# Kernel optimization log

Hardware: AMD Instinct MI355X
Metric: run time of the kernel (lower is better)

## Reference

```python
import jax, jax.numpy as jnp
import numpy as np

G = 64  # fixed grid size hardcoded in the torch module

def setup_inputs() -> dict:
    key = jax.random.key(0)
    ks = jax.random.split(key, 12)
    N, H = 500000, 256
    s = lambda fan_in: 1.0 / np.sqrt(fan_in)
    return {
        "positions": jax.random.normal(ks[0], (N, 3), jnp.float32) * 2.0,
        "grid_points": jax.random.normal(ks[1], (G, 3), jnp.float32) * 2.0,
        "W1": jax.random.normal(ks[2], (3, 64), jnp.float32) * s(3),
        "b1": jnp.zeros((64,), jnp.float32),
        "W2": jax.random.normal(ks[3], (64, 128), jnp.float32) * s(64),
        "b2": jnp.zeros((128,), jnp.float32),
        "W3": jax.random.normal(ks[4], (128, H), jnp.float32) * s(128),
        "b3": jnp.zeros((H,), jnp.float32),
        "Wn1": jax.random.normal(ks[5], (H, H), jnp.float32) * s(H),
        "bn1": jnp.zeros((H,), jnp.float32),
        "Wn2": jax.random.normal(ks[6], (H, H), jnp.float32) * s(H),
        "bn2": jnp.zeros((H,), jnp.float32),
        "Wh1": jax.random.normal(ks[7], (4, H, 128), jnp.float32) * s(H),
        "bh1": jnp.zeros((4, 128), jnp.float32),
        "Wh2": jax.random.normal(ks[8], (4, 128, 1), jnp.float32) * s(128),
        "bh2": jnp.zeros((4, 1), jnp.float32),
    }

def reference(positions, grid_points, W1, b1, W2, b2, W3, b3,
              Wn1, bn1, Wn2, bn2, Wh1, bh1, Wh2, bh2):
    # crystal_encoder: per-atom MLP 3 -> 64 -> 128 -> 256 over ALL N atoms
    h = jax.nn.relu(positions @ W1 + b1)
    h = jax.nn.relu(h @ W2 + b2)
    feat = h @ W3 + b3                                   # [N, H]

    # _map_crystal_to_grid: only the first min(N, 64) atoms are mapped.
    pos64 = positions[:G]                                # [64, 3]
    d2 = jnp.sum((pos64[:, None, :] - grid_points[None, :, :]) ** 2, axis=-1)
    idx = jnp.argmin(d2, axis=-1)                        # [64] nearest grid point per atom
    winner = jnp.full((G,), -1, jnp.int32).at[idx].max(jnp.arange(G, dtype=jnp.int32))
    grid_feats = jnp.where(winner[:, None] >= 0,
                           feat[jnp.clip(winner, 0)], 0.0)  # [64, H]

    # TetrahedralAGINetwork (per-node MLP, channels-first output convention)
    x = grid_feats[None]                                 # [1, 64, H]
    y = jax.nn.relu(x @ Wn1 + bn1) @ Wn2 + bn2           # [1, 64, H]
    agg = jnp.mean(jnp.swapaxes(y, 1, 2), axis=-1)       # mean over nodes -> [1, H]

    # 4 property heads, batched: [4, 1, 1] -> [4] (order: band_gap,
    # elastic_modulus, thermal_conductivity, dielectric_constant)
    h1 = jax.nn.relu(jnp.einsum('bc,kcd->kbd', agg, Wh1) + bh1[:, None, :])
    props = jnp.einsum('kbd,kdo->kbo', h1, Wh2) + bh2[:, None, :]
    return props.reshape(4)
```

## Files before the change

### kernel.cpp

```cpp
#include <hip/hip_runtime.h>


__device__ __forceinline__ void async_cp16(const float* g, float* l) {
    __builtin_amdgcn_global_load_lds(
        (const __attribute__((address_space(1))) void*)g,
        (__attribute__((address_space(3))) void*)l, 16, 0, 0);
}
__device__ __forceinline__ void stage_contig(const float* g, float* l, int nfloats, int tid) {
    const int lane = tid & 63, wv = tid >> 6;
    const int ninst = nfloats >> 8;
    for (int i = wv; i < ninst; i += 4)
        async_cp16(g + i*256 + lane*4, l + i*256);
}
__device__ __forceinline__ void stage_slice32(const float* g, float* l, int ld, int j0, int nrows, int tid) {
    const int lane = tid & 63, wv = tid >> 6;
    const int r = lane >> 3, c4 = (lane & 7) << 2;
    const int ninst = nrows >> 3;
    for (int i = wv; i < ninst; i += 4)
        async_cp16(g + (i*8 + r)*ld + j0 + c4, l + i*256);
}
__device__ __forceinline__ void stage_slice16(const float* g, float* l, int ld, int j0, int nrows, int tid) {
    const int lane = tid & 63, wv = tid >> 6;
    const int r = lane >> 2, c4 = (lane & 3) << 2;
    const int ninst = nrows >> 4;
    for (int i = wv; i < ninst; i += 4)
        async_cp16(g + (i*16 + r)*ld + j0 + c4, l + i*256);
}

__global__ __launch_bounds__(256) void k1a_gf(
    const float* __restrict__ positions, const float* __restrict__ grid_pts,
    const float* __restrict__ W1, const float* __restrict__ b1,
    const float* __restrict__ W2, const float* __restrict__ b2,
    const float* __restrict__ W3, const float* __restrict__ b3,
    float* __restrict__ gf_ws)
{
    __shared__ __align__(16) float w3s[128*32];
    __shared__ float pos_s[192], grid_s[192], w1_s[192], b1_s[64];
    __shared__ int   idx_s[64], win_s[8];
    __shared__ __align__(16) float h1s[8*64];
    __shared__ __align__(16) float h2s[8*128];

    const int tid = threadIdx.x;
    const int blk = blockIdx.x;
    const int bg  = blk >> 3;
    const int j0  = (blk & 7) * 32;

    if (tid < 192) { pos_s[tid] = positions[tid]; grid_s[tid] = grid_pts[tid]; w1_s[tid] = W1[tid]; }
    if (tid >= 192) b1_s[tid - 192] = b1[tid - 192];
    const float bb2 = b2[tid & 127];
    __syncthreads();

    stage_slice32(W3, w3s, 256, j0, 128, tid);
    if (tid < 64) {
        const float px = pos_s[tid*3], py = pos_s[tid*3+1], pz = pos_s[tid*3+2];
        float best = 3.4e38f; int bi = 0;
        for (int g = 0; g < 64; ++g) {
            const float dx = px - grid_s[g*3];
            const float dy = py - grid_s[g*3+1];
            const float dz = pz - grid_s[g*3+2];
            const float d2 = dx*dx + dy*dy + dz*dz;
            if (d2 < best) { best = d2; bi = g; }
        }
        idx_s[tid] = bi;
    }
    __syncthreads();
    if (tid < 8) {
        const int g = bg*8 + tid;
        int m = -1;
        for (int i = 0; i < 64; ++i) if (idx_s[i] == g) m = i;
        win_s[tid] = m;
    }
    __syncthreads();

    #pragma unroll
    for (int u = 0; u < 2; ++u) {
        const int e  = tid + u*256;
        const int lr = e >> 6, kk = e & 63;
        int r = win_s[lr]; if (r < 0) r = 0;
        const float acc = b1_s[kk] + pos_s[r*3]*w1_s[kk] + pos_s[r*3+1]*w1_s[64+kk]
                                   + pos_s[r*3+2]*w1_s[128+kk];
        h1s[lr*64 + kk] = fmaxf(acc, 0.f);
    }
    __syncthreads();

    {
        const int d = tid & 127, t0 = tid >> 7;
        float acc[4];
        #pragma unroll
        for (int m = 0; m < 4; ++m) acc[m] = bb2;
        for (int kc = 0; kc < 64; kc += 16) {
            float w[16];
            #pragma unroll
            for (int u = 0; u < 16; ++u) w[u] = W2[(kc+u)*128 + d];
            #pragma unroll
            for (int u = 0; u < 16; u += 4) {
                #pragma unroll
                for (int m = 0; m < 4; ++m) {
                    const float4 h4 = *(const float4*)&h1s[(t0 + 2*m)*64 + kc + u];
                    acc[m] += h4.x*w[u] + h4.y*w[u+1] + h4.z*w[u+2] + h4.w*w[u+3];
                }
            }
        }
        #pragma unroll
        for (int m = 0; m < 4; ++m)
            h2s[(t0 + 2*m)*128 + d] = fmaxf(acc[m], 0.f);
    }
    __syncthreads();

    {
        const int t = tid >> 5, jl = tid & 31;
        float ag = 0.f;
        for (int dc = 0; dc < 128; dc += 16) {
            float w[16];
            #pragma unroll
            for (int u = 0; u < 16; ++u) w[u] = w3s[(dc+u)*32 + jl];
            #pragma unroll
            for (int u = 0; u < 16; u += 4) {
                const float4 h4 = *(const float4*)&h2s[t*128 + dc + u];
                ag += h4.x*w[u] + h4.y*w[u+1] + h4.z*w[u+2] + h4.w*w[u+3];
            }
        }
        const float bb3 = b3[j0 + jl];
        gf_ws[(bg*8 + t)*256 + j0 + jl] = (win_s[t] >= 0) ? (ag + bb3) : 0.f;
    }
}

__global__ __launch_bounds__(256) void k1b_tpart(
    const float* __restrict__ Wn1, const float* __restrict__ bn1,
    const float* __restrict__ gf_ws, float* __restrict__ tpart_ws)
{
    __shared__ __align__(16) float wn1_s[256*16];
    __shared__ __align__(16) float gf_s[8*256];
    __shared__ float r_s[128];

    const int tid = threadIdx.x;
    const int bg  = blockIdx.x >> 4;
    const int j0  = (blockIdx.x & 15) * 16;
    stage_slice16(Wn1, wn1_s, 256, j0, 256, tid);
    stage_contig(gf_ws + bg*8*256, gf_s, 8*256, tid);

    const int jl = tid & 15, t = tid >> 4;
    const float bb = bn1[j0 + jl];
    __syncthreads();

    if (t < 8) {
        float acc = bb;
        for (int cc = 0; cc < 256; cc += 32) {
            float w[32];
            #pragma unroll
            for (int u = 0; u < 32; ++u) w[u] = wn1_s[(cc+u)*16 + jl];
            #pragma unroll
            for (int u = 0; u < 32; u += 4) {
                const float4 g4 = *(const float4*)&gf_s[t*256 + cc + u];
                acc += g4.x*w[u] + g4.y*w[u+1] + g4.z*w[u+2] + g4.w*w[u+3];
            }
        }
        r_s[t*16 + jl] = fmaxf(acc, 0.f);
    }
    __syncthreads();
    if (t == 0) {
        float ps = 0.f;
        #pragma unroll
        for (int tt = 0; tt < 8; ++tt) ps += r_s[tt*16 + jl];
        tpart_ws[bg*256 + j0 + jl] = ps;
    }
}

__global__ __launch_bounds__(256) void k2_agg(
    const float* __restrict__ Wn2, const float* __restrict__ bn2,
    const float* __restrict__ tpart_ws, float* __restrict__ agg_ws,
    unsigned int* __restrict__ cnts)
{
    __shared__ __align__(16) float wn2_s[256*8];
    __shared__ __align__(16) float tp_s[2048];
    __shared__ __align__(16) float tbar_s[256];

    const int tid = threadIdx.x;
    const int j0a = blockIdx.x * 8;

    if (blockIdx.x == 0 && tid == 0) cnts[0] = 0u;
    {
        const int lane = tid & 63, wv = tid >> 6;
        const int r = lane >> 1, c4 = (lane & 1) << 2;
        for (int i = wv; i < 8; i += 4)
            async_cp16(Wn2 + (i*32 + r)*256 + j0a + c4, wn2_s + i*256);
    }
    stage_contig(tpart_ws, tp_s, 2048, tid);
    __syncthreads();

    {
        float tb = 0.f;
        #pragma unroll
        for (int q = 0; q < 8; ++q) tb += tp_s[q*256 + tid];
        tbar_s[tid] = tb * (1.f/64.f);
    }
    __syncthreads();

    if (tid < 8) {
        float acc = bn2[j0a + tid];
        for (int jc = 0; jc < 256; jc += 32) {
            float w[32];
            #pragma unroll
            for (int u = 0; u < 32; ++u) w[u] = wn2_s[(jc+u)*8 + tid];
            #pragma unroll
            for (int u = 0; u < 32; u += 4) {
                const float4 t4 = *(const float4*)&tbar_s[jc + u];
                acc += t4.x*w[u] + t4.y*w[u+1] + t4.z*w[u+2] + t4.w*w[u+3];
            }
        }
        agg_ws[j0a + tid] = acc;
    }
}

__global__ __launch_bounds__(256) void k34_h1out(
    const float* __restrict__ Wh1, const float* __restrict__ bh1,
    const float* __restrict__ Wh2, const float* __restrict__ bh2,
    const float* __restrict__ agg_ws, float* __restrict__ h1h_ws,
    unsigned int* __restrict__ cnts, float* __restrict__ out)
{
    __shared__ __align__(16) float whs[256*32];
    __shared__ __align__(16) float agg_s[256];
    __shared__ int last_s;

    const int tid = threadIdx.x;
    const int k   = blockIdx.x >> 2;
    const int d0  = (blockIdx.x & 3) * 32;

    stage_slice32(Wh1 + k*32768, whs, 128, d0, 256, tid);
    agg_s[tid] = agg_ws[tid];
    __syncthreads();

    if (tid < 32) {
        const int dl = tid;
        float a = bh1[k*128 + d0 + dl];
        for (int cc = 0; cc < 256; cc += 16) {
            float wa[16];
            #pragma unroll
            for (int u = 0; u < 16; ++u) wa[u] = whs[(cc+u)*32 + dl];
            #pragma unroll
            for (int u = 0; u < 16; u += 4) {
                const float4 a4 = *(const float4*)&agg_s[cc + u];
                a += a4.x*wa[u] + a4.y*wa[u+1] + a4.z*wa[u+2] + a4.w*wa[u+3];
            }
        }
        h1h_ws[k*128 + d0 + dl] = fmaxf(a, 0.f);
    }
    __threadfence();
    __syncthreads();
    if (tid == 0) {
        const unsigned old = __hip_atomic_fetch_add(
            &cnts[0], 1u, __ATOMIC_ACQ_REL, __HIP_MEMORY_SCOPE_AGENT);
        last_s = (old == 15u) ? 1 : 0;
    }
    __syncthreads();
    if (last_s && tid < 4) {
        const int kk = tid;
        float a = bh2[kk];
        for (int d = 0; d < 128; ++d)
            a += h1h_ws[kk*128 + d] * Wh2[kk*128 + d];
        out[kk] = a;
    }
}

extern "C" void kernel_launch(void* const* d_in, const int* in_sizes, int n_in,
                              void* d_out, int out_size, void* d_ws, size_t ws_size,
                              hipStream_t stream) {
    const float* positions = (const float*)d_in[0];
    const float* grid      = (const float*)d_in[1];
    const float* W1  = (const float*)d_in[2];
    const float* b1  = (const float*)d_in[3];
    const float* W2  = (const float*)d_in[4];
    const float* b2  = (const float*)d_in[5];
    const float* W3  = (const float*)d_in[6];
    const float* b3  = (const float*)d_in[7];
    const float* Wn1 = (const float*)d_in[8];
    const float* bn1 = (const float*)d_in[9];
    const float* Wn2 = (const float*)d_in[10];
    const float* bn2 = (const float*)d_in[11];
    const float* Wh1 = (const float*)d_in[12];
    const float* bh1 = (const float*)d_in[13];
    const float* Wh2 = (const float*)d_in[14];
    const float* bh2 = (const float*)d_in[15];
    float* out = (float*)d_out;

    char* ws = (char*)d_ws;
    float* gf_ws    = (float*)(ws + 0);
    float* tpart_ws = (float*)(ws + 65536);
    float* agg_ws   = (float*)(ws + 73728);
    float* h1h_ws   = (float*)(ws + 74752);
    unsigned int* cnts = (unsigned int*)(ws + 76800);

    hipLaunchKernelGGL(k1a_gf,    dim3(64),  dim3(256), 0, stream,
                       positions, grid, W1, b1, W2, b2, W3, b3, gf_ws);
    hipLaunchKernelGGL(k1b_tpart, dim3(128), dim3(256), 0, stream,
                       Wn1, bn1, gf_ws, tpart_ws);
    hipLaunchKernelGGL(k2_agg,    dim3(32),  dim3(256), 0, stream,
                       Wn2, bn2, tpart_ws, agg_ws, cnts);
    hipLaunchKernelGGL(k34_h1out, dim3(16),  dim3(256), 0, stream,
                       Wh1, bh1, Wh2, bh2, agg_ws, h1h_ws, cnts, out);
}
```

Before: 104.1 us.

## Fuse four stage kernels into one persistent kernel with atomic counter barriers

Replaces the four separate kernel launches with a single 240-block kernel. Blocks are partitioned by index into the four stages, and each stage waits on a global atomic counter published by the stage before it. Weight slices are prefetched into LDS before each wait, so weight loading overlaps the upstream stage and three launch gaps go away. It adds a memset launch to reset the counters. Correctness relies on every block being co-resident, and a spin guard breaks out of the wait after a bounded number of iterations, which could let a stage read stale data.

```diff
diff --git a/kernel.cpp b/kernel.cpp
--- a/kernel.cpp
+++ b/kernel.cpp
@@ -27,238 +27,263 @@
         async_cp16(g + (i*16 + r)*ld + j0 + c4, l + i*256);
 }
 
-__global__ __launch_bounds__(256) void k1a_gf(
+#define SPIN_GUARD (1u << 22)
+__device__ __forceinline__ void wait_cnt(unsigned int* p, unsigned int target) {
+    unsigned int g = 0;
+    while (__hip_atomic_load(p, __ATOMIC_ACQUIRE, __HIP_MEMORY_SCOPE_AGENT) < target) {
+        if (++g > SPIN_GUARD) break;
+    }
+}
+
+__global__ __launch_bounds__(256) void mega(
     const float* __restrict__ positions, const float* __restrict__ grid_pts,
     const float* __restrict__ W1, const float* __restrict__ b1,
     const float* __restrict__ W2, const float* __restrict__ b2,
     const float* __restrict__ W3, const float* __restrict__ b3,
-    float* __restrict__ gf_ws)
+    const float* __restrict__ Wn1, const float* __restrict__ bn1,
+    const float* __restrict__ Wn2, const float* __restrict__ bn2,
+    const float* __restrict__ Wh1, const float* __restrict__ bh1,
+    const float* __restrict__ Wh2, const float* __restrict__ bh2,
+    float* __restrict__ gf_ws, float* __restrict__ tpart_ws,
+    float* __restrict__ agg_ws, float* __restrict__ h1h_ws,
+    unsigned int* __restrict__ cnts, float* __restrict__ out)
 {
-    __shared__ __align__(16) float w3s[128*32];
-    __shared__ float pos_s[192], grid_s[192], w1_s[192], b1_s[64];
-    __shared__ int   idx_s[64], win_s[8];
-    __shared__ __align__(16) float h1s[8*64];
-    __shared__ __align__(16) float h2s[8*128];
-
     const int tid = threadIdx.x;
     const int blk = blockIdx.x;
-    const int bg  = blk >> 3;
-    const int j0  = (blk & 7) * 32;
-
-    if (tid < 192) { pos_s[tid] = positions[tid]; grid_s[tid] = grid_pts[tid]; w1_s[tid] = W1[tid]; }
-    if (tid >= 192) b1_s[tid - 192] = b1[tid - 192];
-    const float bb2 = b2[tid & 127];
-    __syncthreads();
-
-    stage_slice32(W3, w3s, 256, j0, 128, tid);
-    if (tid < 64) {
-        const float px = pos_s[tid*3], py = pos_s[tid*3+1], pz = pos_s[tid*3+2];
-        float best = 3.4e38f; int bi = 0;
-        for (int g = 0; g < 64; ++g) {
-            const float dx = px - grid_s[g*3];
-            const float dy = py - grid_s[g*3+1];
-            const float dz = pz - grid_s[g*3+2];
-            const float d2 = dx*dx + dy*dy + dz*dz;
-            if (d2 < best) { best = d2; bi = g; }
-        }
-        idx_s[tid] = bi;
-    }
-    __syncthreads();
-    if (tid < 8) {
-        const int g = bg*8 + tid;
-        int m = -1;
-        for (int i = 0; i < 64; ++i) if (idx_s[i] == g) m = i;
-        win_s[tid] = m;
-    }
-    __syncthreads();
-
-    #pragma unroll
-    for (int u = 0; u < 2; ++u) {
-        const int e  = tid + u*256;
-        const int lr = e >> 6, kk = e & 63;
-        int r = win_s[lr]; if (r < 0) r = 0;
-        const float acc = b1_s[kk] + pos_s[r*3]*w1_s[kk] + pos_s[r*3+1]*w1_s[64+kk]
-                                   + pos_s[r*3+2]*w1_s[128+kk];
-        h1s[lr*64 + kk] = fmaxf(acc, 0.f);
-    }
-    __syncthreads();
+
+    if (blk < 64) {
+        __shared__ __align__(16) float w3s[128*32];
+        __shared__ float pos_s[192], grid_s[192], w1_s[192], b1_s[64];
+        __shared__ int   idx_s[64], win_s[8];
+        __shared__ __align__(16) float h1s[8*64];
+        __shared__ __align__(16) float h2s[8*128];
+
+        const int bg = blk >> 3;
+        const int j0 = (blk & 7) * 32;
+
+        if (tid < 192) { pos_s[tid] = positions[tid]; grid_s[tid] = grid_pts[tid]; w1_s[tid] = W1[tid]; }
+        if (tid >= 192) b1_s[tid - 192] = b1[tid - 192];
+        const float bb2 = b2[tid & 127];
+        __syncthreads();
+
+        stage_slice32(W3, w3s, 256, j0, 128, tid);
+        if (tid < 64) {
+            const float px = pos_s[tid*3], py = pos_s[tid*3+1], pz = pos_s[tid*3+2];
+            float best = 3.4e38f; int bi = 0;
+            for (int g = 0; g < 64; ++g) {
+                const float dx = px - grid_s[g*3];
+                const float dy = py - grid_s[g*3+1];
+                const float dz = pz - grid_s[g*3+2];
+                const float d2 = dx*dx + dy*dy + dz*dz;
+                if (d2 < best) { best = d2; bi = g; }
+            }
+            idx_s[tid] = bi;
+        }
+        __syncthreads();
+        if (tid < 8) {
+            const int g = bg*8 + tid;
+            int m = -1;
+            for (int i = 0; i < 64; ++i) if (idx_s[i] == g) m = i;
+            win_s[tid] = m;
+        }
+        __syncthreads();
+
+        #pragma unroll
+        for (int u = 0; u < 2; ++u) {
+            const int e  = tid + u*256;
+            const int lr = e >> 6, kk = e & 63;
+            int r = win_s[lr]; if (r < 0) r = 0;
+            const float acc = b1_s[kk] + pos_s[r*3]*w1_s[kk] + pos_s[r*3+1]*w1_s[64+kk]
+                                       + pos_s[r*3+2]*w1_s[128+kk];
+            h1s[lr*64 + kk] = fmaxf(acc, 0.f);
+        }
+        __syncthreads();
+
+        {
+            const int d = tid & 127, t0 = tid >> 7;
+            float acc[4];
+            #pragma unroll
+            for (int m = 0; m < 4; ++m) acc[m] = bb2;
+            for (int kc = 0; kc < 64; kc += 16) {
+                float w[16];
+                #pragma unroll
+                for (int u = 0; u < 16; ++u) w[u] = W2[(kc+u)*128 + d];
+                #pragma unroll
+                for (int u = 0; u < 16; u += 4) {
+                    #pragma unroll
+                    for (int m = 0; m < 4; ++m) {
+                        const float4 h4 = *(const float4*)&h1s[(t0 + 2*m)*64 + kc + u];
+                        acc[m] += h4.x*w[u] + h4.y*w[u+1] + h4.z*w[u+2] + h4.w*w[u+3];
+                    }
+                }
+            }
+            #pragma unroll
+            for (int m = 0; m < 4; ++m)
+                h2s[(t0 + 2*m)*128 + d] = fmaxf(acc[m], 0.f);
+        }
+        __syncthreads();
+
+        {
+            const int t = tid >> 5, jl = tid & 31;
+            float ag = 0.f;
+            for (int dc = 0; dc < 128; dc += 16) {
+                float w[16];
+                #pragma unroll
+                for (int u = 0; u < 16; ++u) w[u] = w3s[(dc+u)*32 + jl];
+                #pragma unroll
+                for (int u = 0; u < 16; u += 4) {
+                    const float4 h4 = *(const float4*)&h2s[t*128 + dc + u];
+                    ag += h4.x*w[u] + h4.y*w[u+1] + h4.z*w[u+2] + h4.w*w[u+3];
+                }
+            }
+            const float bb3 = b3[j0 + jl];
+            gf_ws[(bg*8 + t)*256 + j0 + jl] = (win_s[t] >= 0) ? (ag + bb3) : 0.f;
+        }
+        __threadfence();
+        __syncthreads();
+        if (tid == 0)
+            __hip_atomic_fetch_add(&cnts[0], 1u, __ATOMIC_RELEASE, __HIP_MEMORY_SCOPE_AGENT);
+        return;
+    }
+
+    if (blk < 192) {
+        __shared__ __align__(16) float wn1_s[256*16];
+        __shared__ __align__(16) float gf_s[8*256];
+        __shared__ float r_s[128];
+
+        const int b2i = blk - 64;
+        const int bg  = b2i >> 4;
+        const int j0  = (b2i & 15) * 16;
+        stage_slice16(Wn1, wn1_s, 256, j0, 256, tid);
+
+        if (tid == 0) wait_cnt(&cnts[0], 64u);
+        __syncthreads();
+        stage_contig(gf_ws + bg*8*256, gf_s, 8*256, tid);
+
+        const int jl = tid & 15, t = tid >> 4;
+        const float bb = bn1[j0 + jl];
+        __syncthreads();
+
+        if (t < 8) {
+            float acc = bb;
+            for (int cc = 0; cc < 256; cc += 32) {
+                float w[32];
+                #pragma unroll
+                for (int u = 0; u < 32; ++u) w[u] = wn1_s[(cc+u)*16 + jl];
+                #pragma unroll
+                for (int u = 0; u < 32; u += 4) {
+                    const float4 g4 = *(const float4*)&gf_s[t*256 + cc + u];
+                    acc += g4.x*w[u] + g4.y*w[u+1] + g4.z*w[u+2] + g4.w*w[u+3];
+                }
+            }
+            r_s[t*16 + jl] = fmaxf(acc, 0.f);
+        }
+        __syncthreads();
+        if (t == 0) {
+            float ps = 0.f;
+            #pragma unroll
+            for (int tt = 0; tt < 8; ++tt) ps += r_s[tt*16 + jl];
+            tpart_ws[bg*256 + j0 + jl] = ps;
+        }
+        __threadfence();
+        __syncthreads();
+        if (tid == 0)
+            __hip_atomic_fetch_add(&cnts[1], 1u, __ATOMIC_RELEASE, __HIP_MEMORY_SCOPE_AGENT);
+        return;
+    }
+
+    if (blk < 224) {
+        __shared__ __align__(16) float wn2_s[256*8];
+        __shared__ __align__(16) float tp_s[2048];
+        __shared__ __align__(16) float tbar_s[256];
+
+        const int j0a = (blk - 192) * 8;
+
+        {
+            const int lane = tid & 63, wv = tid >> 6;
+            const int r = lane >> 1, c4 = (lane & 1) << 2;
+            for (int i = wv; i < 8; i += 4)
+                async_cp16(Wn2 + (i*32 + r)*256 + j0a + c4, wn2_s + i*256);
+        }
+        if (tid == 0) wait_cnt(&cnts[1], 128u);
+        __syncthreads();
+        stage_contig(tpart_ws, tp_s, 2048, tid);
+        __syncthreads();
+
+        {
+            float tb = 0.f;
+            #pragma unroll
+            for (int q = 0; q < 8; ++q) tb += tp_s[q*256 + tid];
+            tbar_s[tid] = tb * (1.f/64.f);
+        }
+        __syncthreads();
+
+        if (tid < 8) {
+            float acc = bn2[j0a + tid];
+            for (int jc = 0; jc < 256; jc += 32) {
+                float w[32];
+                #pragma unroll
+                for (int u = 0; u < 32; ++u) w[u] = wn2_s[(jc+u)*8 + tid];
+                #pragma unroll
+                for (int u = 0; u < 32; u += 4) {
+                    const float4 t4 = *(const float4*)&tbar_s[jc + u];
+                    acc += t4.x*w[u] + t4.y*w[u+1] + t4.z*w[u+2] + t4.w*w[u+3];
+                }
+            }
+            agg_ws[j0a + tid] = acc;
+        }
+        __threadfence();
+        __syncthreads();
+        if (tid == 0)
+            __hip_atomic_fetch_add(&cnts[2], 1u, __ATOMIC_RELEASE, __HIP_MEMORY_SCOPE_AGENT);
+        return;
+    }
 
     {
-        const int d = tid & 127, t0 = tid >> 7;
-        float acc[4];
-        #pragma unroll
-        for (int m = 0; m < 4; ++m) acc[m] = bb2;
-        for (int kc = 0; kc < 64; kc += 16) {
-            float w[16];
-            #pragma unroll
-            for (int u = 0; u < 16; ++u) w[u] = W2[(kc+u)*128 + d];
-            #pragma unroll
-            for (int u = 0; u < 16; u += 4) {
-                #pragma unroll
-                for (int m = 0; m < 4; ++m) {
-                    const float4 h4 = *(const float4*)&h1s[(t0 + 2*m)*64 + kc + u];
-                    acc[m] += h4.x*w[u] + h4.y*w[u+1] + h4.z*w[u+2] + h4.w*w[u+3];
-                }
-            }
-        }
-        #pragma unroll
-        for (int m = 0; m < 4; ++m)
-            h2s[(t0 + 2*m)*128 + d] = fmaxf(acc[m], 0.f);
-    }
-    __syncthreads();
-
-    {
-        const int t = tid >> 5, jl = tid & 31;
-        float ag = 0.f;
-        for (int dc = 0; dc < 128; dc += 16) {
-            float w[16];
-            #pragma unroll
-            for (int u = 0; u < 16; ++u) w[u] = w3s[(dc+u)*32 + jl];
-            #pragma unroll
-            for (int u = 0; u < 16; u += 4) {
-                const float4 h4 = *(const float4*)&h2s[t*128 + dc + u];
-                ag += h4.x*w[u] + h4.y*w[u+1] + h4.z*w[u+2] + h4.w*w[u+3];
-            }
-        }
-        const float bb3 = b3[j0 + jl];
-        gf_ws[(bg*8 + t)*256 + j0 + jl] = (win_s[t] >= 0) ? (ag + bb3) : 0.f;
-    }
-}
-
-__global__ __launch_bounds__(256) void k1b_tpart(
-    const float* __restrict__ Wn1, const float* __restrict__ bn1,
-    const float* __restrict__ gf_ws, float* __restrict__ tpart_ws)
-{
-    __shared__ __align__(16) float wn1_s[256*16];
-    __shared__ __align__(16) float gf_s[8*256];
-    __shared__ float r_s[128];
-
-    const int tid = threadIdx.x;
-    const int bg  = blockIdx.x >> 4;
-    const int j0  = (blockIdx.x & 15) * 16;
-    stage_slice16(Wn1, wn1_s, 256, j0, 256, tid);
-    stage_contig(gf_ws + bg*8*256, gf_s, 8*256, tid);
-
-    const int jl = tid & 15, t = tid >> 4;
-    const float bb = bn1[j0 + jl];
-    __syncthreads();
-
-    if (t < 8) {
-        float acc = bb;
-        for (int cc = 0; cc < 256; cc += 32) {
-            float w[32];
-            #pragma unroll
-            for (int u = 0; u < 32; ++u) w[u] = wn1_s[(cc+u)*16 + jl];
-            #pragma unroll
-            for (int u = 0; u < 32; u += 4) {
-                const float4 g4 = *(const float4*)&gf_s[t*256 + cc + u];
-                acc += g4.x*w[u] + g4.y*w[u+1] + g4.z*w[u+2] + g4.w*w[u+3];
-            }
-        }
-        r_s[t*16 + jl] = fmaxf(acc, 0.f);
-    }
-    __syncthreads();
-    if (t == 0) {
-        float ps = 0.f;
-        #pragma unroll
-        for (int tt = 0; tt < 8; ++tt) ps += r_s[tt*16 + jl];
-        tpart_ws[bg*256 + j0 + jl] = ps;
-    }
-}
-
-__global__ __launch_bounds__(256) void k2_agg(
-    const float* __restrict__ Wn2, const float* __restrict__ bn2,
-    const float* __restrict__ tpart_ws, float* __restrict__ agg_ws,
-    unsigned int* __restrict__ cnts)
-{
-    __shared__ __align__(16) float wn2_s[256*8];
-    __shared__ __align__(16) float tp_s[2048];
-    __shared__ __align__(16) float tbar_s[256];
-
-    const int tid = threadIdx.x;
-    const int j0a = blockIdx.x * 8;
-
-    if (blockIdx.x == 0 && tid == 0) cnts[0] = 0u;
-    {
-        const int lane = tid & 63, wv = tid >> 6;
-        const int r = lane >> 1, c4 = (lane & 1) << 2;
-        for (int i = wv; i < 8; i += 4)
-            async_cp16(Wn2 + (i*32 + r)*256 + j0a + c4, wn2_s + i*256);
-    }
-    stage_contig(tpart_ws, tp_s, 2048, tid);
-    __syncthreads();
-
-    {
-        float tb = 0.f;
-        #pragma unroll
-        for (int q = 0; q < 8; ++q) tb += tp_s[q*256 + tid];
-        tbar_s[tid] = tb * (1.f/64.f);
-    }
-    __syncthreads();
-
-    if (tid < 8) {
-        float acc = bn2[j0a + tid];
-        for (int jc = 0; jc < 256; jc += 32) {
-            float w[32];
-            #pragma unroll
-            for (int u = 0; u < 32; ++u) w[u] = wn2_s[(jc+u)*8 + tid];
-            #pragma unroll
-            for (int u = 0; u < 32; u += 4) {
-                const float4 t4 = *(const float4*)&tbar_s[jc + u];
-                acc += t4.x*w[u] + t4.y*w[u+1] + t4.z*w[u+2] + t4.w*w[u+3];
-            }
-        }
-        agg_ws[j0a + tid] = acc;
-    }
-}
-
-__global__ __launch_bounds__(256) void k34_h1out(
-    const float* __restrict__ Wh1, const float* __restrict__ bh1,
-    const float* __restrict__ Wh2, const float* __restrict__ bh2,
-    const float* __restrict__ agg_ws, float* __restrict__ h1h_ws,
-    unsigned int* __restrict__ cnts, float* __restrict__ out)
-{
-    __shared__ __align__(16) float whs[256*32];
-    __shared__ __align__(16) float agg_s[256];
-    __shared__ int last_s;
-
-    const int tid = threadIdx.x;
-    const int k   = blockIdx.x >> 2;
-    const int d0  = (blockIdx.x & 3) * 32;
-
-    stage_slice32(Wh1 + k*32768, whs, 128, d0, 256, tid);
-    agg_s[tid] = agg_ws[tid];
-    __syncthreads();
-
-    if (tid < 32) {
-        const int dl = tid;
-        float a = bh1[k*128 + d0 + dl];
-        for (int cc = 0; cc < 256; cc += 16) {
-            float wa[16];
-            #pragma unroll
-            for (int u = 0; u < 16; ++u) wa[u] = whs[(cc+u)*32 + dl];
-            #pragma unroll
-            for (int u = 0; u < 16; u += 4) {
-                const float4 a4 = *(const float4*)&agg_s[cc + u];
-                a += a4.x*wa[u] + a4.y*wa[u+1] + a4.z*wa[u+2] + a4.w*wa[u+3];
-            }
-        }
-        h1h_ws[k*128 + d0 + dl] = fmaxf(a, 0.f);
-    }
-    __threadfence();
-    __syncthreads();
-    if (tid == 0) {
-        const unsigned old = __hip_atomic_fetch_add(
-            &cnts[0], 1u, __ATOMIC_ACQ_REL, __HIP_MEMORY_SCOPE_AGENT);
-        last_s = (old == 15u) ? 1 : 0;
-    }
-    __syncthreads();
-    if (last_s && tid < 4) {
-        const int kk = tid;
-        float a = bh2[kk];
-        for (int d = 0; d < 128; ++d)
-            a += h1h_ws[kk*128 + d] * Wh2[kk*128 + d];
-        out[kk] = a;
+        __shared__ __align__(16) float whs[256*32];
+        __shared__ __align__(16) float agg_s[256];
+        __shared__ int last_s;
+
+        const int hb = blk - 224;
+        const int k  = hb >> 2;
+        const int d0 = (hb & 3) * 32;
+
+        stage_slice32(Wh1 + k*32768, whs, 128, d0, 256, tid);
+        if (tid == 0) wait_cnt(&cnts[2], 32u);
+        __syncthreads();
+        agg_s[tid] = agg_ws[tid];
+        __syncthreads();
+
+        if (tid < 32) {
+            const int dl = tid;
+            float a = bh1[k*128 + d0 + dl];
+            for (int cc = 0; cc < 256; cc += 16) {
+                float wa[16];
+                #pragma unroll
+                for (int u = 0; u < 16; ++u) wa[u] = whs[(cc+u)*32 + dl];
+                #pragma unroll
+                for (int u = 0; u < 16; u += 4) {
+                    const float4 a4 = *(const float4*)&agg_s[cc + u];
+                    a += a4.x*wa[u] + a4.y*wa[u+1] + a4.z*wa[u+2] + a4.w*wa[u+3];
+                }
+            }
+            h1h_ws[k*128 + d0 + dl] = fmaxf(a, 0.f);
+        }
+        __threadfence();
+        __syncthreads();
+        if (tid == 0) {
+            const unsigned old = __hip_atomic_fetch_add(
+                &cnts[3], 1u, __ATOMIC_ACQ_REL, __HIP_MEMORY_SCOPE_AGENT);
+            last_s = (old == 15u) ? 1 : 0;
+        }
+        __syncthreads();
+        if (last_s && tid < 4) {
+            const int kk = tid;
+            float a = bh2[kk];
+            for (int d = 0; d < 128; ++d)
+                a += h1h_ws[kk*128 + d] * Wh2[kk*128 + d];
+            out[kk] = a;
+        }
     }
 }
 
@@ -281,7 +306,7 @@
     const float* bh1 = (const float*)d_in[13];
     const float* Wh2 = (const float*)d_in[14];
     const float* bh2 = (const float*)d_in[15];
-    float* out = (float*)d_out;
+    float* outp = (float*)d_out;
 
     char* ws = (char*)d_ws;
     float* gf_ws    = (float*)(ws + 0);
@@ -290,12 +315,10 @@
     float* h1h_ws   = (float*)(ws + 74752);
     unsigned int* cnts = (unsigned int*)(ws + 76800);
 
-    hipLaunchKernelGGL(k1a_gf,    dim3(64),  dim3(256), 0, stream,
-                       positions, grid, W1, b1, W2, b2, W3, b3, gf_ws);
-    hipLaunchKernelGGL(k1b_tpart, dim3(128), dim3(256), 0, stream,
-                       Wn1, bn1, gf_ws, tpart_ws);
-    hipLaunchKernelGGL(k2_agg,    dim3(32),  dim3(256), 0, stream,
-                       Wn2, bn2, tpart_ws, agg_ws, cnts);
-    hipLaunchKernelGGL(k34_h1out, dim3(16),  dim3(256), 0, stream,
-                       Wh1, bh1, Wh2, bh2, agg_ws, h1h_ws, cnts, out);
-}
+    (void)hipMemsetAsync((void*)cnts, 0, 16, stream);
+
+    hipLaunchKernelGGL(mega, dim3(240), dim3(256), 0, stream,
+                       positions, grid, W1, b1, W2, b2, W3, b3,
+                       Wn1, bn1, Wn2, bn2, Wh1, bh1, Wh2, bh2,
+                       gf_ws, tpart_ws, agg_ws, h1h_ws, cnts, outp);
+}
```

After: 150.5 us. +44.6%, slower.
